# Kernel optimization log

Measured on AMD Instinct MI355X. Metric: run time of the kernel, lower is better.

## Reference

```python
import jax, jax.numpy as jnp
import numpy as np

B, L, D, C = 16, 1444, 128, 21  # batch, graph_len (38*38), feature dim, num_classes


def setup_inputs() -> dict:
    key = jax.random.key(0)
    k1, k2, k3 = jax.random.split(key, 3)
    cls_r_prob = jax.random.uniform(k1, (C, C), dtype=jnp.float32)
    source = jax.random.normal(k2, (B, L, D), dtype=jnp.float32)
    class_idx = jax.random.randint(k3, (B, L), 0, C, dtype=jnp.int64)
    return {"cls_r_prob": cls_r_prob, "source": source, "class_idx": class_idx}


def reference(cls_r_prob, source, class_idx):
    # Vectorized build_local_graph:
    # torch loop sets graph[n,i,j] = P[ci, cj] for j < i, then adds its transpose
    # and an identity whose diagonal is zeroed where class_idx == 0.
    G = cls_r_prob[class_idx[:, :, None], class_idx[:, None, :]]  # [B, L, L] pairwise gather
    M = jnp.tril(G, -1)                                           # strict lower triangle
    graph = M + jnp.swapaxes(M, 1, 2)                             # symmetrize
    ar = jnp.arange(L)
    diag = (class_idx != 0).astype(source.dtype)                  # [B, L]
    graph = graph.at[:, ar, ar].add(diag)                         # masked identity
    # bmm aggregation: fused_buffer = graph @ source
    fused = jnp.einsum('bij,bjd->bid', graph, source)             # [B, L, D]
    return fused, source
```

## Files before the change

kernel.cpp:

```cpp
#include <hip/hip_runtime.h>

#define BB 16
#define LL 1444
#define DD 128
#define CC 21
#define CH 38
#define NK 38
#define RH 19
#define KK (CH + 2*CC)

#define CS_ELEMS ((size_t)BB*NK*CC*DD)

#define ASG __attribute__((address_space(1)))
#define ASL __attribute__((address_space(3)))

static __device__ __forceinline__ void gll16(const float* g, float* l) {
  __builtin_amdgcn_global_load_lds((const ASG void*)g, (ASL void*)l, 16, 0, 0);
}
static __device__ __forceinline__ void gll4(const float* g, float* l) {
  __builtin_amdgcn_global_load_lds((const ASG void*)g, (ASL void*)l, 4, 0, 0);
}

__global__ __launch_bounds__(256) void k1_chunk_sums(
    const float* __restrict__ src, const int* __restrict__ idx,
    float* __restrict__ cs, float* __restrict__ src_copy)
{
  __shared__ __align__(16) float Vs[CH][DD];
  int tid = threadIdx.x;
  int w = tid >> 6, lane = tid & 63;
  int b = blockIdx.x / NK, kc = blockIdx.x % NK;
  int i0 = kc * CH;
  const float* sc = src + (size_t)(b * LL + i0) * DD;

  for (int i = w; i < 19; i += 4)
    gll16(sc + i * 256 + lane * 4, &Vs[0][0] + i * 256);
  __syncthreads();

  const int* gidx = idx + b * LL + i0;
  int d = tid & 127;
  int c0 = (tid >> 7) * 10;
  float acc[11];
#pragma unroll
  for (int j = 0; j < 11; ++j) acc[j] = 0.f;

#pragma unroll
  for (int t = 0; t < CH; ++t) {
    int ct = gidx[t];
    float v = Vs[t][d];
#pragma unroll
    for (int j = 0; j < 11; ++j) {
      float m = (ct == c0 + j) ? 1.0f : 0.0f;
      acc[j] += m * v;
    }
  }

  float* co = cs + ((size_t)(b * NK + kc) * CC) * DD + d;
#pragma unroll
  for (int j = 0; j < 11; ++j) co[(c0 + j) * DD] = acc[j];

  const float4* v4 = (const float4*)&Vs[0][0];
  float4* o4 = (float4*)(src_copy + (size_t)(b * LL + i0) * DD);
  for (int i = tid; i < CH * DD / 4; i += 256) o4[i] = v4[i];
}

__global__ __launch_bounds__(128) void k2_scan(
    float* __restrict__ cs, float* __restrict__ tot)
{
  int b = blockIdx.x / CC, c = blockIdx.x % CC;
  int d = threadIdx.x;
  float* base = cs + ((size_t)(b * NK) * CC + c) * DD + d;
  const int S = CC * DD;
  float a[RH];
  float run = 0.f;
#pragma unroll
  for (int i = 0; i < RH; ++i) a[i] = base[(size_t)i * S];
#pragma unroll
  for (int i = 0; i < RH; ++i) { float t = a[i]; base[(size_t)i * S] = run; run += t; }
#pragma unroll
  for (int i = 0; i < RH; ++i) a[i] = base[(size_t)(RH + i) * S];
#pragma unroll
  for (int i = 0; i < RH; ++i) { float t = a[i]; base[(size_t)(RH + i) * S] = run; run += t; }
  tot[((size_t)(b * CC + c)) * DD + d] = run;
}

#define GEMM_BODY(kv)                                                   \
  {                                                                     \
    float x = X[(kv)][d];                                               \
    const float4* gp = (const float4*)(Gh + (kv) * 20);                 \
    float4 g0 = gp[0], g1 = gp[1], g2 = gp[2], g3 = gp[3], g4 = gp[4];  \
    acc[0]  += g0.x * x; acc[1]  += g0.y * x; acc[2]  += g0.z * x;      \
    acc[3]  += g0.w * x; acc[4]  += g1.x * x; acc[5]  += g1.y * x;      \
    acc[6]  += g1.z * x; acc[7]  += g1.w * x; acc[8]  += g2.x * x;      \
    acc[9]  += g2.y * x; acc[10] += g2.z * x; acc[11] += g2.w * x;      \
    acc[12] += g3.x * x; acc[13] += g3.y * x; acc[14] += g3.z * x;      \
    acc[15] += g3.w * x; acc[16] += g4.x * x; acc[17] += g4.y * x;      \
    acc[18] += g4.z * x;                                                \
  }

__global__ __launch_bounds__(256) void k4_fused(
    const float* __restrict__ src, const int* __restrict__ idx,
    const float* __restrict__ P, const float* __restrict__ cs,
    const float* __restrict__ tot, float* __restrict__ out)
{
  __shared__ __align__(16) float X[KK][DD];
  __shared__ __align__(16) float GA[KK][20];
  __shared__ __align__(16) float GB[KK][20];

  int tid = threadIdx.x;
  int w = tid >> 6, lane = tid & 63;
  int b = blockIdx.x / NK, kc = blockIdx.x % NK;
  int i0 = kc * CH;

  const float* sc = src + (size_t)(b * LL + i0) * DD;
  const float* pc = cs + ((size_t)(b * NK + kc) * CC) * DD;
  const float* tb = tot + (size_t)b * CC * DD;
  float* xf = &X[0][0];

  for (int i = w; i < 19; i += 4) gll16(sc + i * 256 + lane * 4, xf + i * 256);
  for (int i = w; i < 10; i += 4) gll16(pc + i * 256 + lane * 4, xf + CH * DD + i * 256);
  for (int i = w; i < 10; i += 4) gll16(tb + i * 256 + lane * 4, xf + (CH + CC) * DD + i * 256);
  if (w < 2) gll4(pc + 2560 + w * 64 + lane, xf + CH * DD + 2560 + w * 64);
  else       gll4(tb + 2560 + (w - 2) * 64 + lane, xf + (CH + CC) * DD + 2560 + (w - 2) * 64);

  const int* gidx = idx + b * LL + i0;
  for (int e = tid; e < 2 * KK * 20; e += 256) {
    int h = e / (KK * 20);
    int rem = e - h * (KK * 20);
    int k = rem / 20, j = rem - k * 20;
    int t = h * RH + j;
    float val = 0.f;
    if (j < RH) {
      int ct = gidx[t];
      if (k < CH) {
        if (k < t) { int ck = gidx[k]; val = P[ct * CC + ck] - P[ck * CC + ct]; }
        else if (k == t) val = (ct != 0 ? 1.0f : 0.0f) - P[ct * CC + ct];
      } else if (k < CH + CC) {
        int c = k - CH; val = P[ct * CC + c] - P[c * CC + ct];
      } else {
        int c = k - CH - CC; val = P[c * CC + ct];
      }
    }
    (h ? &GB[0][0] : &GA[0][0])[k * 20 + j] = val;
  }
  __syncthreads();

  int rw = __builtin_amdgcn_readfirstlane(w >> 1);
  int dh = w & 1;
  int d = dh * 64 + lane;
  const float* Gh = rw ? &GB[0][0] : &GA[0][0];

  float acc[RH];
#pragma unroll
  for (int j = 0; j < RH; ++j) acc[j] = 0.f;

  int kend1 = __builtin_amdgcn_readfirstlane(rw ? CH : RH);
  for (int k = 0; k < kend1; ++k) GEMM_BODY(k)
  for (int k = CH; k < KK; ++k)   GEMM_BODY(k)

  float* op = out + (size_t)(b * LL + i0 + rw * RH) * DD + d;
#pragma unroll
  for (int j = 0; j < RH; ++j) op[(size_t)j * DD] = acc[j];
}

extern "C" void kernel_launch(void* const* d_in, const int* in_sizes, int n_in,
                              void* d_out, int out_size, void* d_ws, size_t ws_size,
                              hipStream_t stream) {
  const float* P   = (const float*)d_in[0];
  const float* src = (const float*)d_in[1];
  const int*   idx = (const int*)d_in[2];

  float* out_fused = (float*)d_out;
  float* out_src   = out_fused + (size_t)BB * LL * DD;

  float* cs  = (float*)d_ws;
  float* tot = cs + CS_ELEMS;

  k1_chunk_sums<<<BB * NK, 256, 0, stream>>>(src, idx, cs, out_src);
  k2_scan<<<BB * CC, 128, 0, stream>>>(cs, tot);
  k4_fused<<<BB * NK, 256, 0, stream>>>(src, idx, P, cs, tot, out_fused);
}
```

Measured before the change: 103.2 us.

## Fuse three kernels into one cooperative kernel with grid syncs

Replaces the three launches (chunk sums, scan, fused GEMM) with a single cooperative kernel of 608 blocks of 128 threads. Two grid-wide barriers separate the phases, and the per-chunk prefix and total rows are read from global memory into registers rather than staged in LDS. This removes launch gaps and redundant reloads of the source tile, but halves the threads per block, so each thread now does both row halves serially. It also adds grid.sync overhead and relies on all blocks being co-resident, falling back to the old path otherwise.

```diff
diff --git a/kernel.cpp b/kernel.cpp
--- a/kernel.cpp
+++ b/kernel.cpp
@@ -1,4 +1,7 @@
 #include <hip/hip_runtime.h>
+#include <hip/hip_cooperative_groups.h>
+
+namespace cg = cooperative_groups;
 
 #define BB 16
 #define LL 1444
@@ -19,6 +22,147 @@
 }
 static __device__ __forceinline__ void gll4(const float* g, float* l) {
   __builtin_amdgcn_global_load_lds((const ASG void*)g, (ASL void*)l, 4, 0, 0);
+}
+
+#define GEMM_BODY_X(kv, xv)                                             \
+  {                                                                     \
+    float x = (xv);                                                     \
+    const float4* gp = (const float4*)(Gh + (kv) * 20);                 \
+    float4 g0 = gp[0], g1 = gp[1], g2 = gp[2], g3 = gp[3], g4 = gp[4];  \
+    acc[0]  += g0.x * x; acc[1]  += g0.y * x; acc[2]  += g0.z * x;      \
+    acc[3]  += g0.w * x; acc[4]  += g1.x * x; acc[5]  += g1.y * x;      \
+    acc[6]  += g1.z * x; acc[7]  += g1.w * x; acc[8]  += g2.x * x;      \
+    acc[9]  += g2.y * x; acc[10] += g2.z * x; acc[11] += g2.w * x;      \
+    acc[12] += g3.x * x; acc[13] += g3.y * x; acc[14] += g3.z * x;      \
+    acc[15] += g3.w * x; acc[16] += g4.x * x; acc[17] += g4.y * x;      \
+    acc[18] += g4.z * x;                                                \
+  }
+
+__global__ __launch_bounds__(128, 2) void fused_all(
+    const float* __restrict__ src, const int* __restrict__ idx,
+    const float* __restrict__ P, float* __restrict__ cs,
+    float* __restrict__ tot, float* __restrict__ out,
+    float* __restrict__ src_copy)
+{
+  __shared__ __align__(16) float X[CH][DD];
+  __shared__ __align__(16) float GA[KK][20];
+  __shared__ __align__(16) float GB[KK][20];
+
+  cg::grid_group grid = cg::this_grid();
+
+  int tid = threadIdx.x;
+  int w = tid >> 6, lane = tid & 63;
+  int b = blockIdx.x / NK, kc = blockIdx.x % NK;
+  int i0 = kc * CH;
+  const float* sc = src + (size_t)(b * LL + i0) * DD;
+
+  for (int i = w; i < 19; i += 2)
+    gll16(sc + i * 256 + lane * 4, &X[0][0] + i * 256);
+  __syncthreads();
+
+  const int* gidx = idx + b * LL + i0;
+
+  {
+    int d = tid;
+    float a1[CC];
+#pragma unroll
+    for (int j = 0; j < CC; ++j) a1[j] = 0.f;
+#pragma unroll
+    for (int t = 0; t < CH; ++t) {
+      int ct = gidx[t];
+      float v = X[t][d];
+#pragma unroll
+      for (int j = 0; j < CC; ++j) {
+        float m = (ct == j) ? 1.0f : 0.0f;
+        a1[j] += m * v;
+      }
+    }
+    float* co = cs + ((size_t)(b * NK + kc) * CC) * DD + d;
+#pragma unroll
+    for (int j = 0; j < CC; ++j) co[(size_t)j * DD] = a1[j];
+  }
+
+  {
+    const float4* v4 = (const float4*)&X[0][0];
+    float4* o4 = (float4*)(src_copy + (size_t)(b * LL + i0) * DD);
+    for (int i = tid; i < CH * DD / 4; i += 128) o4[i] = v4[i];
+  }
+
+  for (int e = tid; e < 2 * KK * 20; e += 128) {
+    int h = e / (KK * 20);
+    int rem = e - h * (KK * 20);
+    int k = rem / 20, j = rem - k * 20;
+    int t = h * RH + j;
+    float val = 0.f;
+    if (j < RH) {
+      int ct = gidx[t];
+      if (k < CH) {
+        if (k < t) { int ck = gidx[k]; val = P[ct * CC + ck] - P[ck * CC + ct]; }
+        else if (k == t) val = (ct != 0 ? 1.0f : 0.0f) - P[ct * CC + ct];
+      } else if (k < CH + CC) {
+        int c = k - CH; val = P[ct * CC + c] - P[c * CC + ct];
+      } else {
+        int c = k - CH - CC; val = P[c * CC + ct];
+      }
+    }
+    (h ? &GB[0][0] : &GA[0][0])[k * 20 + j] = val;
+  }
+
+  __threadfence();
+  grid.sync();
+  __threadfence();
+
+  if (blockIdx.x < BB * CC) {
+    int b2 = blockIdx.x / CC, c2 = blockIdx.x % CC;
+    float* base = cs + ((size_t)(b2 * NK) * CC + c2) * DD + tid;
+    const int S = CC * DD;
+    float a[RH];
+    float run = 0.f;
+#pragma unroll
+    for (int i = 0; i < RH; ++i) a[i] = base[(size_t)i * S];
+#pragma unroll
+    for (int i = 0; i < RH; ++i) { float t = a[i]; base[(size_t)i * S] = run; run += t; }
+#pragma unroll
+    for (int i = 0; i < RH; ++i) a[i] = base[(size_t)(RH + i) * S];
+#pragma unroll
+    for (int i = 0; i < RH; ++i) { float t = a[i]; base[(size_t)(RH + i) * S] = run; run += t; }
+    tot[((size_t)(b2 * CC + c2)) * DD + tid] = run;
+  }
+
+  __threadfence();
+  grid.sync();
+  __threadfence();
+
+  {
+    int d = tid;
+    const float* pc = cs + ((size_t)(b * NK + kc) * CC) * DD + d;
+    const float* tb = tot + ((size_t)b * CC) * DD + d;
+    float pr[CC], tr[CC];
+#pragma unroll
+    for (int c = 0; c < CC; ++c) pr[c] = pc[(size_t)c * DD];
+#pragma unroll
+    for (int c = 0; c < CC; ++c) tr[c] = tb[(size_t)c * DD];
+
+#define HALF_ROWS(rwc, GH, KEND)                                        \
+    {                                                                   \
+      const float* Gh = &GH[0][0];                                      \
+      float acc[RH];                                                    \
+      _Pragma("unroll")                                                 \
+      for (int j = 0; j < RH; ++j) acc[j] = 0.f;                        \
+      for (int k = 0; k < (KEND); ++k) GEMM_BODY_X(k, X[k][d])          \
+      _Pragma("unroll")                                                 \
+      for (int c = 0; c < CC; ++c) GEMM_BODY_X(CH + c, pr[c])           \
+      _Pragma("unroll")                                                 \
+      for (int c = 0; c < CC; ++c) GEMM_BODY_X(CH + CC + c, tr[c])      \
+      float* op = out + (size_t)(b * LL + i0 + (rwc) * RH) * DD + d;    \
+      _Pragma("unroll")                                                 \
+      for (int j = 0; j < RH; ++j) op[(size_t)j * DD] = acc[j];         \
+    }
+
+    HALF_ROWS(0, GA, RH)
+    HALF_ROWS(1, GB, CH)
+#undef HALF_ROWS
+  }
 }
 
 __global__ __launch_bounds__(256) void k1_chunk_sums(
@@ -82,20 +226,6 @@
   for (int i = 0; i < RH; ++i) { float t = a[i]; base[(size_t)(RH + i) * S] = run; run += t; }
   tot[((size_t)(b * CC + c)) * DD + d] = run;
 }
-
-#define GEMM_BODY(kv)                                                   \
-  {                                                                     \
-    float x = X[(kv)][d];                                               \
-    const float4* gp = (const float4*)(Gh + (kv) * 20);                 \
-    float4 g0 = gp[0], g1 = gp[1], g2 = gp[2], g3 = gp[3], g4 = gp[4];  \
-    acc[0]  += g0.x * x; acc[1]  += g0.y * x; acc[2]  += g0.z * x;      \
-    acc[3]  += g0.w * x; acc[4]  += g1.x * x; acc[5]  += g1.y * x;      \
-    acc[6]  += g1.z * x; acc[7]  += g1.w * x; acc[8]  += g2.x * x;      \
-    acc[9]  += g2.y * x; acc[10] += g2.z * x; acc[11] += g2.w * x;      \
-    acc[12] += g3.x * x; acc[13] += g3.y * x; acc[14] += g3.z * x;      \
-    acc[15] += g3.w * x; acc[16] += g4.x * x; acc[17] += g4.y * x;      \
-    acc[18] += g4.z * x;                                                \
-  }
 
 __global__ __launch_bounds__(256) void k4_fused(
     const float* __restrict__ src, const int* __restrict__ idx,
@@ -154,8 +284,8 @@
   for (int j = 0; j < RH; ++j) acc[j] = 0.f;
 
   int kend1 = __builtin_amdgcn_readfirstlane(rw ? CH : RH);
-  for (int k = 0; k < kend1; ++k) GEMM_BODY(k)
-  for (int k = CH; k < KK; ++k)   GEMM_BODY(k)
+  for (int k = 0; k < kend1; ++k) GEMM_BODY_X(k, X[k][d])
+  for (int k = CH; k < KK; ++k)   GEMM_BODY_X(k, X[k][d])
 
   float* op = out + (size_t)(b * LL + i0 + rw * RH) * DD + d;
 #pragma unroll
@@ -175,6 +305,25 @@
   float* cs  = (float*)d_ws;
   float* tot = cs + CS_ELEMS;
 
+  static int coop_ok = -1;
+  if (coop_ok < 0) {
+    int dev = 0, ncu = 0, nb = 0;
+    hipError_t e0 = hipGetDevice(&dev);
+    hipError_t e1 = hipDeviceGetAttribute(&ncu, hipDeviceAttributeMultiprocessorCount, dev);
+    hipError_t e2 = hipOccupancyMaxActiveBlocksPerMultiprocessor(&nb, fused_all, 128, 0);
+    coop_ok = (e0 == hipSuccess && e1 == hipSuccess && e2 == hipSuccess &&
+               nb > 0 && (long)nb * (long)ncu >= (long)(BB * NK)) ? 1 : 0;
+  }
+
+  if (coop_ok == 1) {
+    void* args[] = {(void*)&src, (void*)&idx, (void*)&P, (void*)&cs,
+                    (void*)&tot, (void*)&out_fused, (void*)&out_src};
+    hipError_t e = hipLaunchCooperativeKernel((void*)fused_all, dim3(BB * NK),
+                                              dim3(128), args, 0, stream);
+    if (e == hipSuccess) return;
+    coop_ok = 0;
+  }
+
   k1_chunk_sums<<<BB * NK, 256, 0, stream>>>(src, idx, cs, out_src);
   k2_scan<<<BB * CC, 128, 0, stream>>>(cs, tot);
   k4_fused<<<BB * NK, 256, 0, stream>>>(src, idx, P, cs, tot, out_fused);
```

Measured after the change: 101.9 us. Within noise of the previous version (-1.3%).

## Fold prefix-scan kernel into fused GEMM kernel and swizzle blocks across XCDs

Applied to the files above, without the earlier changes.

Removes the separate scan kernel. Each block of the fused kernel now recomputes its own exclusive prefix and total over all chunk sums for its batch by reading the raw per-chunk class sums directly. It also remaps block IDs so that all blocks of a batch land on the same XCD, which should improve L2 reuse of those chunk sums. This drops one launch and a global round trip, but every block now does redundant reads of NK*CC*DD values serially before it can compute.

```diff
diff --git a/kernel.cpp b/kernel.cpp
--- a/kernel.cpp
+++ b/kernel.cpp
@@ -17,9 +17,28 @@
 static __device__ __forceinline__ void gll16(const float* g, float* l) {
   __builtin_amdgcn_global_load_lds((const ASG void*)g, (ASL void*)l, 16, 0, 0);
 }
-static __device__ __forceinline__ void gll4(const float* g, float* l) {
-  __builtin_amdgcn_global_load_lds((const ASG void*)g, (ASL void*)l, 4, 0, 0);
+
+static __device__ __forceinline__ void swz_bkc(int bid, int& b, int& kc) {
+  int xcd = bid & 7;
+  int slot = bid >> 3;
+  int hi = (slot >= NK) ? 1 : 0;
+  b = xcd * 2 + hi;
+  kc = slot - hi * NK;
 }
+
+#define GEMM_BODY_X(kv, xv)                                             \
+  {                                                                     \
+    float x = (xv);                                                     \
+    const float4* gp = (const float4*)(Gh + (kv) * 20);                 \
+    float4 g0 = gp[0], g1 = gp[1], g2 = gp[2], g3 = gp[3], g4 = gp[4];  \
+    acc[0]  += g0.x * x; acc[1]  += g0.y * x; acc[2]  += g0.z * x;      \
+    acc[3]  += g0.w * x; acc[4]  += g1.x * x; acc[5]  += g1.y * x;      \
+    acc[6]  += g1.z * x; acc[7]  += g1.w * x; acc[8]  += g2.x * x;      \
+    acc[9]  += g2.y * x; acc[10] += g2.z * x; acc[11] += g2.w * x;      \
+    acc[12] += g3.x * x; acc[13] += g3.y * x; acc[14] += g3.z * x;      \
+    acc[15] += g3.w * x; acc[16] += g4.x * x; acc[17] += g4.y * x;      \
+    acc[18] += g4.z * x;                                                \
+  }
 
 __global__ __launch_bounds__(256) void k1_chunk_sums(
     const float* __restrict__ src, const int* __restrict__ idx,
@@ -28,7 +47,8 @@
   __shared__ __align__(16) float Vs[CH][DD];
   int tid = threadIdx.x;
   int w = tid >> 6, lane = tid & 63;
-  int b = blockIdx.x / NK, kc = blockIdx.x % NK;
+  int b, kc;
+  swz_bkc(blockIdx.x, b, kc);
   int i0 = kc * CH;
   const float* sc = src + (size_t)(b * LL + i0) * DD;
 
@@ -63,44 +83,10 @@
   for (int i = tid; i < CH * DD / 4; i += 256) o4[i] = v4[i];
 }
 
-__global__ __launch_bounds__(128) void k2_scan(
-    float* __restrict__ cs, float* __restrict__ tot)
-{
-  int b = blockIdx.x / CC, c = blockIdx.x % CC;
-  int d = threadIdx.x;
-  float* base = cs + ((size_t)(b * NK) * CC + c) * DD + d;
-  const int S = CC * DD;
-  float a[RH];
-  float run = 0.f;
-#pragma unroll
-  for (int i = 0; i < RH; ++i) a[i] = base[(size_t)i * S];
-#pragma unroll
-  for (int i = 0; i < RH; ++i) { float t = a[i]; base[(size_t)i * S] = run; run += t; }
-#pragma unroll
-  for (int i = 0; i < RH; ++i) a[i] = base[(size_t)(RH + i) * S];
-#pragma unroll
-  for (int i = 0; i < RH; ++i) { float t = a[i]; base[(size_t)(RH + i) * S] = run; run += t; }
-  tot[((size_t)(b * CC + c)) * DD + d] = run;
-}
-
-#define GEMM_BODY(kv)                                                   \
-  {                                                                     \
-    float x = X[(kv)][d];                                               \
-    const float4* gp = (const float4*)(Gh + (kv) * 20);                 \
-    float4 g0 = gp[0], g1 = gp[1], g2 = gp[2], g3 = gp[3], g4 = gp[4];  \
-    acc[0]  += g0.x * x; acc[1]  += g0.y * x; acc[2]  += g0.z * x;      \
-    acc[3]  += g0.w * x; acc[4]  += g1.x * x; acc[5]  += g1.y * x;      \
-    acc[6]  += g1.z * x; acc[7]  += g1.w * x; acc[8]  += g2.x * x;      \
-    acc[9]  += g2.y * x; acc[10] += g2.z * x; acc[11] += g2.w * x;      \
-    acc[12] += g3.x * x; acc[13] += g3.y * x; acc[14] += g3.z * x;      \
-    acc[15] += g3.w * x; acc[16] += g4.x * x; acc[17] += g4.y * x;      \
-    acc[18] += g4.z * x;                                                \
-  }
-
 __global__ __launch_bounds__(256) void k4_fused(
     const float* __restrict__ src, const int* __restrict__ idx,
     const float* __restrict__ P, const float* __restrict__ cs,
-    const float* __restrict__ tot, float* __restrict__ out)
+    float* __restrict__ out)
 {
   __shared__ __align__(16) float X[KK][DD];
   __shared__ __align__(16) float GA[KK][20];
@@ -108,19 +94,37 @@
 
   int tid = threadIdx.x;
   int w = tid >> 6, lane = tid & 63;
-  int b = blockIdx.x / NK, kc = blockIdx.x % NK;
+  int b, kc;
+  swz_bkc(blockIdx.x, b, kc);
   int i0 = kc * CH;
 
   const float* sc = src + (size_t)(b * LL + i0) * DD;
-  const float* pc = cs + ((size_t)(b * NK + kc) * CC) * DD;
-  const float* tb = tot + (size_t)b * CC * DD;
   float* xf = &X[0][0];
 
   for (int i = w; i < 19; i += 4) gll16(sc + i * 256 + lane * 4, xf + i * 256);
-  for (int i = w; i < 10; i += 4) gll16(pc + i * 256 + lane * 4, xf + CH * DD + i * 256);
-  for (int i = w; i < 10; i += 4) gll16(tb + i * 256 + lane * 4, xf + (CH + CC) * DD + i * 256);
-  if (w < 2) gll4(pc + 2560 + w * 64 + lane, xf + CH * DD + 2560 + w * 64);
-  else       gll4(tb + 2560 + (w - 2) * 64 + lane, xf + (CH + CC) * DD + 2560 + (w - 2) * 64);
+
+  {
+    int d = tid & 127;
+    int c0 = (tid >> 7) * 10;
+    const float* cb = cs + ((size_t)(b * NK) * CC + c0) * DD + d;
+    float pre[11], run[11];
+#pragma unroll
+    for (int c = 0; c < 11; ++c) { pre[c] = 0.f; run[c] = 0.f; }
+    for (int j = 0; j < NK; ++j) {
+      if (j == kc) {
+#pragma unroll
+        for (int c = 0; c < 11; ++c) pre[c] = run[c];
+      }
+#pragma unroll
+      for (int c = 0; c < 11; ++c)
+        run[c] += cb[((size_t)j * CC + c) * DD];
+    }
+#pragma unroll
+    for (int c = 0; c < 11; ++c) {
+      X[CH + c0 + c][d]      = pre[c];
+      X[CH + CC + c0 + c][d] = run[c];
+    }
+  }
 
   const int* gidx = idx + b * LL + i0;
   for (int e = tid; e < 2 * KK * 20; e += 256) {
@@ -154,8 +158,8 @@
   for (int j = 0; j < RH; ++j) acc[j] = 0.f;
 
   int kend1 = __builtin_amdgcn_readfirstlane(rw ? CH : RH);
-  for (int k = 0; k < kend1; ++k) GEMM_BODY(k)
-  for (int k = CH; k < KK; ++k)   GEMM_BODY(k)
+  for (int k = 0; k < kend1; ++k) GEMM_BODY_X(k, X[k][d])
+  for (int k = CH; k < KK; ++k)   GEMM_BODY_X(k, X[k][d])
 
   float* op = out + (size_t)(b * LL + i0 + rw * RH) * DD + d;
 #pragma unroll
@@ -172,10 +176,8 @@
   float* out_fused = (float*)d_out;
   float* out_src   = out_fused + (size_t)BB * LL * DD;
 
-  float* cs  = (float*)d_ws;
-  float* tot = cs + CS_ELEMS;
+  float* cs = (float*)d_ws;
 
   k1_chunk_sums<<<BB * NK, 256, 0, stream>>>(src, idx, cs, out_src);
-  k2_scan<<<BB * CC, 128, 0, stream>>>(cs, tot);
-  k4_fused<<<BB * NK, 256, 0, stream>>>(src, idx, P, cs, tot, out_fused);
+  k4_fused<<<BB * NK, 256, 0, stream>>>(src, idx, P, cs, out_fused);
 }
```

Result: slower. 112.9 us (+9.4%).
